# Performance work log

Hardware: AMD Instinct MI355X
Metric: run time of the kernel (lower is better)

The kernel has to match this reference:

```python
import jax, jax.numpy as jnp
import numpy as np

EPS = 1e-12


def setup_inputs() -> dict:
    key = jax.random.key(0)
    k1, k2, k3 = jax.random.split(key, 3)
    n, in_dim, out_dim, R = 4096, 128, 128, 8
    X = jax.random.normal(k1, (n, in_dim), dtype=jnp.float32)
    A = jax.random.uniform(k2, (R, n, n), dtype=jnp.float32)
    # glorot-style scale for weights [R, out_dim, in_dim]
    scale = jnp.sqrt(6.0 / (in_dim + out_dim)).astype(jnp.float32)
    W = jax.random.uniform(k3, (R, out_dim, in_dim), minval=-1.0, maxval=1.0, dtype=jnp.float32) * scale
    return {"X": X, "A": A, "W": W}


def reference(X, A, W):
    # H[r] = X @ W[r].T  -> [R, n, out]
    H = jnp.einsum("nd,rod->rno", X, W)
    # message aggregation per relation: A[r] @ H[r] -> [R, n, out]
    M = jnp.einsum("rmn,rno->rmo", A, H)
    # row-sum degree normalization per relation (detached in original; same value in fwd)
    norms = jnp.sum(A, axis=-1, keepdims=True) + EPS  # [R, n, 1]
    out = jnp.sum(M / norms, axis=0)  # [n, out]
    return out  # activation is Identity
```

## Files before the change

kernel.cpp:

```cpp
#include <hip/hip_runtime.h>


#define N_NODES 4096
#define DIM     128
#define NREL    8
#define EPS_F   1e-12f
#define BM      64
#define BK      64
#define NKT     (N_NODES / BK)
#define TILE_SHORTS (DIM * BK)

typedef __attribute__((ext_vector_type(4))) float f32x4;
typedef __attribute__((ext_vector_type(8))) short bf16x8;

__device__ __forceinline__ unsigned short f2bf(float f) {
  unsigned u = __float_as_uint(f);
  return (unsigned short)((u + 0x7fffu + ((u >> 16) & 1u)) >> 16);
}

__device__ __forceinline__ bf16x8 cvt8(const float* p) {
  f32x4 lo = *reinterpret_cast<const f32x4*>(p);
  f32x4 hi = *reinterpret_cast<const f32x4*>(p + 4);
  bf16x8 o;
#pragma unroll
  for (int j = 0; j < 4; ++j) { o[j] = (short)f2bf(lo[j]); o[j + 4] = (short)f2bf(hi[j]); }
  return o;
}

__device__ __forceinline__ void gload_lds16(const void* g, void* l) {
  __builtin_amdgcn_global_load_lds((const __attribute__((address_space(1))) void*)g,
                                   (__attribute__((address_space(3))) void*)l, 16, 0, 0);
}

__global__ __launch_bounds__(256) void h_kernel(const float* __restrict__ X,
                                                const float* __restrict__ W,
                                                short* __restrict__ Ht2) {
  const int r  = blockIdx.x >> 5;
  const int n0 = (blockIdx.x & 31) * 128;
  const int lane = threadIdx.x & 63;
  const int wid  = threadIdx.x >> 6;
  const int wm = wid >> 1, wn = wid & 1;
  const int l15 = lane & 15, l4 = lane >> 4;

  const float* Wr = W + (size_t)r * DIM * DIM;
  f32x4 acc[4][4] = {};

#pragma unroll
  for (int ks = 0; ks < 4; ++ks) {
    const int k = ks * 32 + l4 * 8;
    bf16x8 a[4], b[4];
#pragma unroll
    for (int mi = 0; mi < 4; ++mi)
      a[mi] = cvt8(Wr + (size_t)(wm * 64 + mi * 16 + l15) * DIM + k);
#pragma unroll
    for (int ni = 0; ni < 4; ++ni)
      b[ni] = cvt8(X + (size_t)(n0 + wn * 64 + ni * 16 + l15) * DIM + k);
#pragma unroll
    for (int mi = 0; mi < 4; ++mi)
#pragma unroll
      for (int ni = 0; ni < 4; ++ni)
        acc[mi][ni] = __builtin_amdgcn_mfma_f32_16x16x32_bf16(a[mi], b[ni], acc[mi][ni], 0, 0, 0);
  }

#pragma unroll
  for (int mi = 0; mi < 4; ++mi)
#pragma unroll
    for (int ni = 0; ni < 4; ++ni)
#pragma unroll
      for (int i = 0; i < 4; ++i) {
        const int o = wm * 64 + mi * 16 + l4 * 4 + i;
        const int n = n0 + wn * 64 + ni * 16 + l15;
        const int kt = n >> 6, c = n & 63;
        Ht2[(size_t)(r * NKT + kt) * TILE_SHORTS + o * 64 + (c ^ ((o & 7) << 3))] =
            (short)f2bf(acc[mi][ni][i]);
      }
}

__global__ __launch_bounds__(256, 2) void rgcn_main(const float* __restrict__ A,
                                                    const short* __restrict__ Ht2,
                                                    float* __restrict__ out) {
  const int nwg = gridDim.x;
  const int logical = (blockIdx.x & 7) * (nwg >> 3) + (blockIdx.x >> 3);
  const int r  = logical >> 6;
  const int m0 = (logical & 63) * BM;

  const int lane = threadIdx.x & 63;
  const int w    = threadIdx.x >> 6;
  const int l15  = lane & 15, l4 = lane >> 4;

  __shared__ __align__(128) short Hs[4][TILE_SHORTS];

  const float* Arow = A + ((size_t)r * N_NODES + m0 + w * 16 + l15) * N_NODES + l4 * 8;
  const short* Hg   = Ht2 + (size_t)r * NKT * TILE_SHORTS + w * 4 * 512 + lane * 8;
  short* lds0 = &Hs[0][0] + w * 2048;
  short* lds1 = &Hs[1][0] + w * 2048;
  short* lds2 = &Hs[2][0] + w * 2048;
  short* lds3 = &Hs[3][0] + w * 2048;

  f32x4 acc[8] = {};
  f32x4 a0[2][2], a1[2][2], a2[2][2], a3[2][2];
  float rs = 0.f;

  auto stage = [&](short* ldsb, int kt) {
    const short* g = Hg + (size_t)kt * TILE_SHORTS;
#pragma unroll
    for (int j = 0; j < 4; ++j)
      gload_lds16(g + j * 512, ldsb + j * 512);
  };
  auto loadA = [&](f32x4 (&d)[2][2], int kt) {
    const float* p = Arow + kt * BK;
    d[0][0] = *reinterpret_cast<const f32x4*>(p);
    d[0][1] = *reinterpret_cast<const f32x4*>(p + 4);
    d[1][0] = *reinterpret_cast<const f32x4*>(p + 32);
    d[1][1] = *reinterpret_cast<const f32x4*>(p + 36);
  };

  const char* hbase = (const char*)&Hs[0][0] + (size_t)l15 * 128;
  const int swz = (l15 & 7) << 4;
  auto compute = [&](int buf, f32x4 (&av)[2][2]) {
    const char* hb = hbase + (size_t)buf * (TILE_SHORTS * 2);
#pragma unroll
    for (int ks = 0; ks < 2; ++ks) {
      bf16x8 ab;
#pragma unroll
      for (int j = 0; j < 4; ++j) {
        ab[j]     = (short)f2bf(av[ks][0][j]);
        ab[j + 4] = (short)f2bf(av[ks][1][j]);
        rs += av[ks][0][j] + av[ks][1][j];
      }
      const int cb = ks * 64 + l4 * 16;
#pragma unroll
      for (int ni = 0; ni < 8; ++ni) {
        bf16x8 h = *reinterpret_cast<const bf16x8*>(hb + ni * 2048 + (cb ^ swz));
        acc[ni] = __builtin_amdgcn_mfma_f32_16x16x32_bf16(ab, h, acc[ni], 0, 0, 0);
      }
    }
  };

#define VMW(N) do { __builtin_amdgcn_sched_barrier(0);                      \
    asm volatile("s_waitcnt vmcnt(" #N ")" ::: "memory");                   \
    __builtin_amdgcn_sched_barrier(0); } while (0)

#define PH(C, P, KT) do {                                                   \
    stage(lds##P, KT); loadA(a##P, KT);                                     \
    VMW(16);                                                                \
    __builtin_amdgcn_s_barrier();                                           \
    compute(C, a##C); } while (0)

  stage(lds0, 0); loadA(a0, 0);
  stage(lds1, 1); loadA(a1, 1);

  for (int t = 0; t < NKT - 4; t += 4) {
    PH(0, 2, t + 2);
    PH(1, 3, t + 3);
    PH(2, 0, t + 4);
    PH(3, 1, t + 5);
  }
  PH(0, 2, 62);
  PH(1, 3, 63);
  VMW(8);  __builtin_amdgcn_s_barrier(); compute(2, a2);
  VMW(0);  __builtin_amdgcn_s_barrier(); compute(3, a3);

#undef PH
#undef VMW

  rs += __shfl_xor(rs, 16);
  rs += __shfl_xor(rs, 32);
  float ninv[4];
#pragma unroll
  for (int i = 0; i < 4; ++i)
    ninv[i] = 1.0f / (__shfl(rs, l4 * 4 + i) + EPS_F);

  float* orow = out + (size_t)(m0 + w * 16) * DIM;
#pragma unroll
  for (int ni = 0; ni < 8; ++ni)
#pragma unroll
    for (int i = 0; i < 4; ++i)
      atomicAdd(&orow[(size_t)(l4 * 4 + i) * DIM + ni * 16 + l15], acc[ni][i] * ninv[i]);
}

extern "C" void kernel_launch(void* const* d_in, const int* in_sizes, int n_in,
                              void* d_out, int out_size, void* d_ws, size_t ws_size,
                              hipStream_t stream) {
  const float* X = (const float*)d_in[0];
  const float* A = (const float*)d_in[1];
  const float* W = (const float*)d_in[2];
  float* out = (float*)d_out;
  short* Ht2 = (short*)d_ws;

  hipMemsetAsync(d_out, 0, (size_t)out_size * sizeof(float), stream);
  hipLaunchKernelGGL(h_kernel, dim3(NREL * (N_NODES / 128)), dim3(256), 0, stream, X, W, Ht2);
  hipLaunchKernelGGL(rgcn_main, dim3(NREL * (N_NODES / BM)), dim3(256), 0, stream, A, Ht2, out);
}
```

Baseline: 159.7 us.

## Use 128-row tiles with split-K pairs and cross-block norm reduction

Each block now covers 128 rows instead of 64, so every wave runs two MFMA row fragments against each staged H tile. This halves H tile traffic per row. The K dimension is split in two across paired blocks, which keeps the grid at 512 blocks. Row sums go through global atomics, and a spin-wait counter makes both halves wait until the full norm is known before they scale and atomically add their outputs. In exchange, double buffering replaces the previous four-stage buffering, two extra barriers are added per phase, and the spin-wait risks deadlock if paired blocks are not co-resident.

Result: slower. 297.5 us (+86.3%).

```diff
diff --git a/kernel.cpp b/kernel.cpp
--- a/kernel.cpp
+++ b/kernel.cpp
@@ -5,9 +5,11 @@
 #define DIM     128
 #define NREL    8
 #define EPS_F   1e-12f
-#define BM      64
+#define BMR     128
 #define BK      64
-#define NKT     (N_NODES / BK)
+#define KSPL    2
+#define PHASES  32
+#define NKT     64
 #define TILE_SHORTS (DIM * BK)
 
 typedef __attribute__((ext_vector_type(4))) float f32x4;
@@ -78,61 +80,74 @@
 
 __global__ __launch_bounds__(256, 2) void rgcn_main(const float* __restrict__ A,
                                                     const short* __restrict__ Ht2,
-                                                    float* __restrict__ out) {
-  const int nwg = gridDim.x;
-  const int logical = (blockIdx.x & 7) * (nwg >> 3) + (blockIdx.x >> 3);
-  const int r  = logical >> 6;
-  const int m0 = (logical & 63) * BM;
-
-  const int lane = threadIdx.x & 63;
-  const int w    = threadIdx.x >> 6;
+                                                    float* __restrict__ out,
+                                                    float* __restrict__ norms,
+                                                    int* __restrict__ counters) {
+  const int logical = (blockIdx.x & 7) * 64 + (blockIdx.x >> 3);
+  const int r   = logical >> 6;
+  const int rem = logical & 63;
+  const int mt  = rem >> 1;
+  const int ksp = rem & 1;
+  const int m0  = mt * BMR;
+  const int cidx = r * 32 + mt;
+
+  const int tid  = threadIdx.x;
+  const int lane = tid & 63;
+  const int w    = tid >> 6;
   const int l15  = lane & 15, l4 = lane >> 4;
 
-  __shared__ __align__(128) short Hs[4][TILE_SHORTS];
-
-  const float* Arow = A + ((size_t)r * N_NODES + m0 + w * 16 + l15) * N_NODES + l4 * 8;
-  const short* Hg   = Ht2 + (size_t)r * NKT * TILE_SHORTS + w * 4 * 512 + lane * 8;
+  __shared__ __align__(128) short Hs[2][TILE_SHORTS];
+
+  const float* Ag = A + ((size_t)r * N_NODES + m0 + w * 32 + l15) * N_NODES
+                      + (size_t)ksp * (N_NODES / KSPL) + l4 * 8;
+  const short* Hgw = Ht2 + (size_t)(r * NKT + ksp * PHASES) * TILE_SHORTS
+                        + w * 2048 + lane * 8;
   short* lds0 = &Hs[0][0] + w * 2048;
   short* lds1 = &Hs[1][0] + w * 2048;
-  short* lds2 = &Hs[2][0] + w * 2048;
-  short* lds3 = &Hs[3][0] + w * 2048;
-
-  f32x4 acc[8] = {};
-  f32x4 a0[2][2], a1[2][2], a2[2][2], a3[2][2];
-  float rs = 0.f;
-
-  auto stage = [&](short* ldsb, int kt) {
-    const short* g = Hg + (size_t)kt * TILE_SHORTS;
+
+  f32x4 acc[2][8] = {};
+  f32x4 a0[2][2][2], a1[2][2][2];
+  float rs[2] = {0.f, 0.f};
+
+  auto stageH = [&](short* ldsb, int t) {
+    const short* g = Hgw + (size_t)t * TILE_SHORTS;
 #pragma unroll
     for (int j = 0; j < 4; ++j)
       gload_lds16(g + j * 512, ldsb + j * 512);
   };
-  auto loadA = [&](f32x4 (&d)[2][2], int kt) {
-    const float* p = Arow + kt * BK;
-    d[0][0] = *reinterpret_cast<const f32x4*>(p);
-    d[0][1] = *reinterpret_cast<const f32x4*>(p + 4);
-    d[1][0] = *reinterpret_cast<const f32x4*>(p + 32);
-    d[1][1] = *reinterpret_cast<const f32x4*>(p + 36);
+  auto loadA = [&](f32x4 (&d)[2][2][2], int t) {
+    const float* p = Ag + (size_t)t * BK;
+#pragma unroll
+    for (int ks = 0; ks < 2; ++ks)
+#pragma unroll
+      for (int mf = 0; mf < 2; ++mf) {
+        const float* q = p + (size_t)mf * 16 * N_NODES + ks * 32;
+        d[ks][mf][0] = *reinterpret_cast<const f32x4*>(q);
+        d[ks][mf][1] = *reinterpret_cast<const f32x4*>(q + 4);
+      }
   };
 
   const char* hbase = (const char*)&Hs[0][0] + (size_t)l15 * 128;
   const int swz = (l15 & 7) << 4;
-  auto compute = [&](int buf, f32x4 (&av)[2][2]) {
+  auto compute = [&](int buf, f32x4 (&av)[2][2][2]) {
     const char* hb = hbase + (size_t)buf * (TILE_SHORTS * 2);
 #pragma unroll
     for (int ks = 0; ks < 2; ++ks) {
-      bf16x8 ab;
-#pragma unroll
-      for (int j = 0; j < 4; ++j) {
-        ab[j]     = (short)f2bf(av[ks][0][j]);
-        ab[j + 4] = (short)f2bf(av[ks][1][j]);
-        rs += av[ks][0][j] + av[ks][1][j];
-      }
+      bf16x8 ab[2];
+#pragma unroll
+      for (int mf = 0; mf < 2; ++mf)
+#pragma unroll
+        for (int j = 0; j < 4; ++j) {
+          ab[mf][j]     = (short)f2bf(av[ks][mf][0][j]);
+          ab[mf][j + 4] = (short)f2bf(av[ks][mf][1][j]);
+          rs[mf] += av[ks][mf][0][j] + av[ks][mf][1][j];
+        }
       const int cb = ks * 64 + l4 * 16;
 #pragma unroll
       for (int ni = 0; ni < 8; ++ni) {
         bf16x8 h = *reinterpret_cast<const bf16x8*>(hb + ni * 2048 + (cb ^ swz));
-        acc[ni] = __builtin_amdgcn_mfma_f32_16x16x32_bf16(ab, h, acc[ni], 0, 0, 0);
+        acc[0][ni] = __builtin_amdgcn_mfma_f32_16x16x32_bf16(ab[0], h, acc[0][ni], 0, 0, 0);
+        acc[1][ni] = __builtin_amdgcn_mfma_f32_16x16x32_bf16(ab[1], h, acc[1][ni], 0, 0, 0);
       }
     }
   };
@@ -140,43 +155,64 @@
 #define VMW(N) do { __builtin_amdgcn_sched_barrier(0);                      \
     asm volatile("s_waitcnt vmcnt(" #N ")" ::: "memory");                   \
     __builtin_amdgcn_sched_barrier(0); } while (0)
-
 #define PH(C, P, KT) do {                                                   \
-    stage(lds##P, KT); loadA(a##P, KT);                                     \
-    VMW(16);                                                                \
+    stageH(lds##P, KT); loadA(a##P, KT);                                    \
+    VMW(12);                                                                \
     __builtin_amdgcn_s_barrier();                                           \
-    compute(C, a##C); } while (0)
-
-  stage(lds0, 0); loadA(a0, 0);
-  stage(lds1, 1); loadA(a1, 1);
-
-  for (int t = 0; t < NKT - 4; t += 4) {
-    PH(0, 2, t + 2);
-    PH(1, 3, t + 3);
-    PH(2, 0, t + 4);
-    PH(3, 1, t + 5);
-  }
-  PH(0, 2, 62);
-  PH(1, 3, 63);
-  VMW(8);  __builtin_amdgcn_s_barrier(); compute(2, a2);
-  VMW(0);  __builtin_amdgcn_s_barrier(); compute(3, a3);
+    compute(C, a##C);                                                       \
+    __builtin_amdgcn_s_barrier(); } while (0)
+
+  stageH(lds0, 0); loadA(a0, 0);
+  for (int s = 0; s < 15; ++s) {
+    PH(0, 1, 2 * s + 1);
+    PH(1, 0, 2 * s + 2);
+  }
+  PH(0, 1, 31);
+  VMW(0);
+  __builtin_amdgcn_s_barrier();
+  compute(1, a1);
 
 #undef PH
 #undef VMW
 
-  rs += __shfl_xor(rs, 16);
-  rs += __shfl_xor(rs, 32);
-  float ninv[4];
-#pragma unroll
-  for (int i = 0; i < 4; ++i)
-    ninv[i] = 1.0f / (__shfl(rs, l4 * 4 + i) + EPS_F);
-
-  float* orow = out + (size_t)(m0 + w * 16) * DIM;
-#pragma unroll
-  for (int ni = 0; ni < 8; ++ni)
-#pragma unroll
-    for (int i = 0; i < 4; ++i)
-      atomicAdd(&orow[(size_t)(l4 * 4 + i) * DIM + ni * 16 + l15], acc[ni][i] * ninv[i]);
+#pragma unroll
+  for (int mf = 0; mf < 2; ++mf) {
+    float s = rs[mf];
+    s += __shfl_xor(s, 16);
+    s += __shfl_xor(s, 32);
+    if (l4 == 0)
+      atomicAdd(&norms[r * N_NODES + m0 + w * 32 + mf * 16 + l15], s);
+  }
+  __threadfence();
+  __syncthreads();
+  if (tid == 0) {
+    atomicAdd(&counters[cidx], 1);
+    while (__hip_atomic_load(&counters[cidx], __ATOMIC_ACQUIRE,
+                             __HIP_MEMORY_SCOPE_AGENT) < KSPL)
+      __builtin_amdgcn_s_sleep(4);
+  }
+  __syncthreads();
+
+  float ninv[2][4];
+#pragma unroll
+  for (int mf = 0; mf < 2; ++mf)
+#pragma unroll
+    for (int i = 0; i < 4; ++i) {
+      float nv = __hip_atomic_load(
+          &norms[r * N_NODES + m0 + w * 32 + mf * 16 + l4 * 4 + i],
+          __ATOMIC_RELAXED, __HIP_MEMORY_SCOPE_AGENT);
+      ninv[mf][i] = 1.0f / (nv + EPS_F);
+    }
+
+  float* orow = out + (size_t)(m0 + w * 32) * DIM;
+#pragma unroll
+  for (int mf = 0; mf < 2; ++mf)
+#pragma unroll
+    for (int ni = 0; ni < 8; ++ni)
+#pragma unroll
+      for (int i = 0; i < 4; ++i)
+        atomicAdd(&orow[(size_t)(mf * 16 + l4 * 4 + i) * DIM + ni * 16 + l15],
+                  acc[mf][ni][i] * ninv[mf][i]);
 }
 
 extern "C" void kernel_launch(void* const* d_in, const int* in_sizes, int n_in,
@@ -186,9 +222,15 @@
   const float* A = (const float*)d_in[1];
   const float* W = (const float*)d_in[2];
   float* out = (float*)d_out;
-  short* Ht2 = (short*)d_ws;
+
+  char* ws = (char*)d_ws;
+  short* Ht2    = (short*)ws;
+  float* norms  = (float*)(ws + (8u << 20));
+  int*   counters = (int*)(ws + (8u << 20) + (128u << 10));
 
   hipMemsetAsync(d_out, 0, (size_t)out_size * sizeof(float), stream);
+  hipMemsetAsync(ws + (8u << 20), 0, (128u << 10) + 1024, stream);
   hipLaunchKernelGGL(h_kernel, dim3(NREL * (N_NODES / 128)), dim3(256), 0, stream, X, W, Ht2);
-  hipLaunchKernelGGL(rgcn_main, dim3(NREL * (N_NODES / BM)), dim3(256), 0, stream, A, Ht2, out);
-}
+  hipLaunchKernelGGL(rgcn_main, dim3(NREL * (N_NODES / BMR) * KSPL), dim3(256), 0, stream,
+                     A, Ht2, out, norms, counters);
+}
```
